# Optimization experiments

Hardware: AMD Instinct MI355X
Metric: run time of the kernel (lower is better)

The kernel has to match this reference:

```python
import jax, jax.numpy as jnp
import numpy as np

NUM_HEADS = 16


def rotate_half(x):
    x1 = x[..., ::2]
    x2 = x[..., 1::2]
    return jnp.concatenate((-x2, x1), axis=-1)


def rope_sin_cos(seq_len, head_dim, dtype):
    inv_freq = 1.0 / (10000.0 ** (jnp.arange(0, head_dim, 2, dtype=jnp.float32) / head_dim))
    t = jnp.arange(seq_len, dtype=jnp.float32)
    freqs = jnp.einsum('i,j->ij', t, inv_freq)          # [S, D/2]
    emb = jnp.concatenate((freqs, freqs), axis=-1)      # [S, D]
    return jnp.sin(emb).astype(dtype), jnp.cos(emb).astype(dtype)


def setup_inputs() -> dict:
    key = jax.random.key(0)
    B, S, E = 2, 2048, 2048
    ks = jax.random.split(key, 5)
    scale = 1.0 / np.sqrt(E)
    return {
        'x': jax.random.normal(ks[0], (B, S, E), dtype=jnp.float32),
        'mask': jnp.ones((B, S), dtype=jnp.int32),
        'Wq': jax.random.normal(ks[1], (E, E), dtype=jnp.float32) * scale,
        'bq': jnp.zeros((E,), dtype=jnp.float32),
        'Wk': jax.random.normal(ks[2], (E, E), dtype=jnp.float32) * scale,
        'bk': jnp.zeros((E,), dtype=jnp.float32),
        'Wv': jax.random.normal(ks[3], (E, E), dtype=jnp.float32) * scale,
        'bv': jnp.zeros((E,), dtype=jnp.float32),
        'Wo': jax.random.normal(ks[4], (E, E), dtype=jnp.float32) * scale,
        'bo': jnp.zeros((E,), dtype=jnp.float32),
    }


def reference(x, mask, Wq, bq, Wk, bk, Wv, bv, Wo, bo):
    B, S, E = x.shape
    H = NUM_HEADS
    D = E // H
    q = (x @ Wq + bq).reshape(B, S, H, D).transpose(0, 2, 1, 3)  # [B,H,S,D]
    k = (x @ Wk + bk).reshape(B, S, H, D).transpose(0, 2, 1, 3)
    v = (x @ Wv + bv).reshape(B, S, H, D).transpose(0, 2, 1, 3)

    sin, cos = rope_sin_cos(S, D, q.dtype)  # [S,D]
    sin = sin[None, None]                    # [1,1,S,D]
    cos = cos[None, None]
    q = q * cos + rotate_half(q) * sin
    k = k * cos + rotate_half(k) * sin

    scores = jnp.einsum('bhqd,bhkd->bhqk', q, k) / jnp.sqrt(jnp.asarray(D, q.dtype))
    scores = jnp.where(mask[:, None, None, :] == 0, -jnp.inf, scores)
    probs = jax.nn.softmax(scores, axis=-1)
    attn = jnp.einsum('bhqk,bhkd->bhqd', probs, v)       # [B,H,S,D]
    attn = attn.transpose(0, 2, 1, 3).reshape(B, S, E)
    return attn @ Wo + bo
```

## Files before the change

### kernel.cpp

```cpp
#include <hip/hip_runtime.h>
#include <hip/hip_bf16.h>
#include <cmath>

typedef unsigned short u16;
typedef unsigned int   u32;

using v4f = __attribute__((ext_vector_type(4))) float;
using s8v = __attribute__((ext_vector_type(8))) short;

union Frag { uint4 u; s8v s; };

__device__ __forceinline__ u16 f2bf(float f){
  u32 u = __float_as_uint(f);
  u32 r = u + 0x7fffu + ((u >> 16) & 1u);
  return (u16)(r >> 16);
}
__device__ __forceinline__ float bf2f(u16 h){ return __uint_as_float(((u32)h) << 16); }

__device__ __forceinline__ void async16(const void* g, void* l){
  __builtin_amdgcn_global_load_lds((__attribute__((address_space(1))) void*)g,
                                   (__attribute__((address_space(3))) void*)l, 16, 0, 0);
}

__global__ __launch_bounds__(256) void cast_x_kernel(const float* __restrict__ x, u16* __restrict__ xb){
  size_t i = ((size_t)blockIdx.x * 256 + threadIdx.x) * 4;
  float4 v = *(const float4*)(x + i);
  uint2 o;
  o.x = (u32)f2bf(v.x) | ((u32)f2bf(v.y) << 16);
  o.y = (u32)f2bf(v.z) | ((u32)f2bf(v.w) << 16);
  *(uint2*)(xb + i) = o;
}

__global__ __launch_bounds__(256) void cast_transpose_kernel(
    const float* __restrict__ W0, const float* __restrict__ W1,
    const float* __restrict__ W2, const float* __restrict__ W3,
    u16* __restrict__ T0, u16* __restrict__ T1, u16* __restrict__ T2, u16* __restrict__ T3){
  __shared__ float tile[64][65];
  const float* W = (blockIdx.z==0)?W0:(blockIdx.z==1)?W1:(blockIdx.z==2)?W2:W3;
  u16*         T = (blockIdx.z==0)?T0:(blockIdx.z==1)?T1:(blockIdx.z==2)?T2:T3;
  const int k0 = blockIdx.y*64, n0 = blockIdx.x*64;
  const int t  = threadIdx.x;
  const int rr = t >> 4, c4 = (t & 15) * 4;
  #pragma unroll
  for (int i=0;i<4;i++){
    int k = rr + i*16;
    float4 v = *(const float4*)(W + (size_t)(k0+k)*2048 + n0 + c4);
    tile[k][c4+0]=v.x; tile[k][c4+1]=v.y; tile[k][c4+2]=v.z; tile[k][c4+3]=v.w;
  }
  __syncthreads();
  #pragma unroll
  for (int i=0;i<4;i++){
    int n = rr + i*16;
    uint2 o;
    o.x = (u32)f2bf(tile[c4+0][n]) | ((u32)f2bf(tile[c4+1][n])<<16);
    o.y = (u32)f2bf(tile[c4+2][n]) | ((u32)f2bf(tile[c4+3][n])<<16);
    *(uint2*)(T + (size_t)(n0+n)*2048 + k0 + c4) = o;
  }
}

template<int MODE>
__global__ __launch_bounds__(256) void gemm_kernel(const u16* __restrict__ A,
                                                   const u16* __restrict__ BT,
                                                   const float* __restrict__ bias,
                                                   void* __restrict__ Cout){
  constexpr int K = 2048;
  __shared__ u16 Asl[128*64];
  __shared__ u16 Bsl[128*64];
  const int tid  = threadIdx.x;
  const int w    = tid >> 6;
  const int lane = tid & 63;
  const int r    = lane & 15, q = lane >> 4;
  const int m0   = blockIdx.y * 128;
  const int n0   = blockIdx.x * 128;
  const int wm   = (w >> 1) * 64, wn = (w & 1) * 64;

  v4f acc[4][4];
  #pragma unroll
  for (int i=0;i<4;i++)
    #pragma unroll
    for (int j=0;j<4;j++) acc[i][j] = (v4f)0.f;

  const int srow = w*32 + (lane>>3);
  const int sblk = (lane&7) ^ ((lane>>3)&7);
  const u16* Ag = A  + (size_t)(m0+srow)*K + sblk*8;
  const u16* Bg = BT + (size_t)(n0+srow)*K + sblk*8;
  u16* Als = Asl + (w*32)*64;
  u16* Bls = Bsl + (w*32)*64;

  for (int kk = 0; kk < K; kk += 64) {
    #pragma unroll
    for (int i=0;i<4;i++){
      async16(Ag + (size_t)i*8*K + kk, Als + i*512);
      async16(Bg + (size_t)i*8*K + kk, Bls + i*512);
    }
    __syncthreads();
    #pragma unroll
    for (int ks=0; ks<2; ++ks) {
      s8v af[4], bfr[4];
      #pragma unroll
      for (int i=0;i<4;i++){
        int rho = wm + i*16 + r;
        int p = (ks*4 + q) ^ (r&7);
        Frag t; t.u = *(const uint4*)(Asl + rho*64 + p*8); af[i] = t.s;
      }
      #pragma unroll
      for (int j=0;j<4;j++){
        int rho = wn + j*16 + r;
        int p = (ks*4 + q) ^ (r&7);
        Frag t; t.u = *(const uint4*)(Bsl + rho*64 + p*8); bfr[j] = t.s;
      }
      #pragma unroll
      for (int i=0;i<4;i++)
        #pragma unroll
        for (int j=0;j<4;j++)
          acc[i][j] = __builtin_amdgcn_mfma_f32_16x16x32_bf16(af[i], bfr[j], acc[i][j], 0, 0, 0);
    }
    __syncthreads();
  }

  float bv[4];
  #pragma unroll
  for (int j=0;j<4;j++) bv[j] = bias[n0 + wn + j*16 + r];

  #pragma unroll
  for (int i=0;i<4;i++){
    #pragma unroll
    for (int j=0;j<4;j++){
      const int gn = n0 + wn + j*16 + r;
      #pragma unroll
      for (int rr2=0; rr2<4; ++rr2){
        const int gm = m0 + wm + i*16 + q*4 + rr2;
        float val = acc[i][j][rr2] + bv[j];
        if (MODE == 0) ((u16*)Cout)[(size_t)gm*2048 + gn] = f2bf(val);
        else           ((float*)Cout)[(size_t)gm*2048 + gn] = val;
      }
    }
  }
}

__global__ __launch_bounds__(256) void rope_kernel(u16* __restrict__ Q, u16* __restrict__ Kb){
  const int wrow = blockIdx.x*4 + (threadIdx.x >> 6);
  const int lane = threadIdx.x & 63;
  u16* P = (blockIdx.y == 0) ? Q : Kb;
  const int s = (wrow >> 4) & 2047;
  const size_t base = (size_t)wrow * 128;
  float invf = exp2f(-(float)lane * 0.20762050593045952f);
  float angle = (float)s * invf;
  float sn, cs;
  sincosf(angle, &sn, &cs);
  float x_j   = bf2f(P[base + lane]);
  float x_j64 = bf2f(P[base + 64 + lane]);
  float x_2j  = bf2f(P[base + 2*lane]);
  float x_2j1 = bf2f(P[base + 2*lane + 1]);
  float o0 = x_j  * cs - x_2j1 * sn;
  float o1 = x_j64 * cs + x_2j  * sn;
  P[base + lane]      = f2bf(o0);
  P[base + 64 + lane] = f2bf(o1);
}

__global__ __launch_bounds__(256) void transpose_v_kernel(const u16* __restrict__ V, u16* __restrict__ VT){
  __shared__ u16 t[64*72];
  const int s0 = blockIdx.x*64;
  const int d0 = blockIdx.y*64;
  const int bh = blockIdx.z;
  const int b = bh >> 4, h = bh & 15;
  const size_t obase = ((size_t)bh*128 + d0)*2048 + s0;
  const int tid = threadIdx.x;
  #pragma unroll
  for (int i=0;i<2;i++){
    int c = tid + i*256;
    int sl = c >> 3, dc = (c & 7) * 8;
    *(uint4*)(t + sl*72 + dc) =
      *(const uint4*)(V + ((size_t)(b*2048 + s0 + sl))*2048 + h*128 + d0 + dc);
  }
  __syncthreads();
  #pragma unroll
  for (int i=0;i<2;i++){
    int c = tid + i*256;
    int dl = c >> 3, sc4 = (c & 7) * 8;
    u16 tmp[8];
    #pragma unroll
    for (int j=0;j<8;j++) tmp[j] = t[(sc4+j)*72 + dl];
    *(uint4*)(VT + obase + (size_t)dl*2048 + sc4) = *(const uint4*)tmp;
  }
}

__global__ __launch_bounds__(256,4) void attn_kernel(const u16* __restrict__ Q,
                                                     const u16* __restrict__ K,
                                                     const u16* __restrict__ VT,
                                                     const int* __restrict__ mask,
                                                     u16* __restrict__ Out){
  constexpr int S = 2048;
  constexpr float SL2 = 0.08838834764831845f * 1.4426950408889634f;
  __shared__ u16 smem[20480];
  u16* KQlds = smem;
  u16* Vlds  = smem + 8192;
  u16* Plds  = smem + 16384;

  const int tid = threadIdx.x, w = tid >> 6, lane = tid & 63;
  const int r = lane & 15, q = lane >> 4;
  const int h = blockIdx.y, b = blockIdx.z;
  const int q0 = blockIdx.x * 64;
  const size_t rowb = (size_t)b * 2048;
  const size_t bhD  = ((size_t)(b*16 + h)) * 128;

  const int sr4 = lane >> 4;
  const int sp16 = lane & 15;
  #pragma unroll
  for (int i=0;i<4;i++){
    int R = w*16 + i*4;
    int blk = sp16 ^ ((R&7) + sr4);
    async16(Q + (rowb + q0 + R + sr4)*2048 + h*128 + blk*8, KQlds + R*128);
  }
  __syncthreads();
  s8v qf[4];
  #pragma unroll
  for (int kc=0;kc<4;kc++){
    int rho = w*16 + r;
    int p = (kc*4 + q) ^ (r&7);
    Frag t; t.u = *(const uint4*)(KQlds + rho*128 + p*8);
    qf[kc] = t.s;
  }
  __syncthreads();

  v4f accO[8];
  #pragma unroll
  for (int n=0;n<8;n++) accO[n] = (v4f)0.f;
  float lsum[4] = {0.f, 0.f, 0.f, 0.f};

  u16* Pw = Plds + w*1024;

  const int vr8 = lane >> 3;
  const int vblk = (lane&7) ^ ((lane>>3)&7);

  for (int it=0; it<32; ++it){
    const int key0 = it*64;
    #pragma unroll
    for (int i=0;i<4;i++){
      int R = w*16 + i*4;
      int blk = sp16 ^ ((R&7) + sr4);
      async16(K + (rowb + key0 + R + sr4)*2048 + h*128 + blk*8, KQlds + R*128);
    }
    #pragma unroll
    for (int i=0;i<4;i++){
      int R = w*32 + i*8;
      async16(VT + (bhD + R + vr8)*2048 + key0 + vblk*8, Vlds + R*64);
    }
    __syncthreads();

    v4f sc[4];
    #pragma unroll
    for (int n=0;n<4;n++){
      v4f a = (v4f)0.f;
      #pragma unroll
      for (int kc=0;kc<4;kc++){
        int rho = n*16 + r;
        int p = (kc*4 + q) ^ (r&7);
        Frag t; t.u = *(const uint4*)(KQlds + rho*128 + p*8);
        a = __builtin_amdgcn_mfma_f32_16x16x32_bf16(qf[kc], t.s, a, 0, 0, 0);
      }
      sc[n] = a;
    }

    int mv[4];
    #pragma unroll
    for (int n=0;n<4;n++) mv[n] = mask[b*S + key0 + n*16 + r];

    #pragma unroll
    for (int g=0;g<4;g++){
      const int row = q*4 + g;
      const int rb = row*64 + (r&7);
      #pragma unroll
      for (int n=0;n<4;n++){
        float p = exp2f(sc[n][g] * SL2);
        if (mv[n] == 0) p = 0.f;
        lsum[g] += p;
        int pp = (n*2 + (r>>3)) ^ (row&7);
        Pw[rb + pp*8] = f2bf(p);
      }
    }

    #pragma unroll
    for (int kc=0;kc<2;kc++){
      int p = (kc*4 + q) ^ (r&7);
      Frag tp; tp.u = *(const uint4*)(Pw + r*64 + p*8);
      #pragma unroll
      for (int n=0;n<8;n++){
        int d = n*16 + r;
        Frag tv; tv.u = *(const uint4*)(Vlds + d*64 + p*8);
        accO[n] = __builtin_amdgcn_mfma_f32_16x16x32_bf16(tp.s, tv.s, accO[n], 0, 0, 0);
      }
    }
    __syncthreads();
  }

  float inv[4];
  #pragma unroll
  for (int g=0;g<4;g++){
    float s = lsum[g];
    #pragma unroll
    for (int off=1; off<16; off<<=1) s += __shfl_xor(s, off, 64);
    inv[g] = (s > 0.f) ? 1.f/s : 0.f;
  }

  #pragma unroll
  for (int n=0;n<8;n++){
    #pragma unroll
    for (int g=0;g<4;g++){
      int s = q0 + w*16 + q*4 + g;
      int col = h*128 + n*16 + r;
      Out[(rowb + s)*2048 + col] = f2bf(accO[n][g] * inv[g]);
    }
  }
}

extern "C" void kernel_launch(void* const* d_in, const int* in_sizes, int n_in,
                              void* d_out, int out_size, void* d_ws, size_t ws_size,
                              hipStream_t stream) {
  (void)in_sizes; (void)n_in; (void)out_size; (void)ws_size;
  const float* x    = (const float*)d_in[0];
  const int*   mask = (const int*)d_in[1];
  const float* Wq   = (const float*)d_in[2];
  const float* bq   = (const float*)d_in[3];
  const float* Wk   = (const float*)d_in[4];
  const float* bk   = (const float*)d_in[5];
  const float* Wv   = (const float*)d_in[6];
  const float* bv   = (const float*)d_in[7];
  const float* Wo   = (const float*)d_in[8];
  const float* bo   = (const float*)d_in[9];

  u16* xbf = (u16*)d_ws;
  u16* WqT = xbf + 8388608;
  u16* WkT = WqT + 4194304;
  u16* WvT = WkT + 4194304;
  u16* WoT = WvT + 4194304;
  u16* Qb  = WoT + 4194304;
  u16* Kb  = Qb + 8388608;
  u16* Vb  = Kb + 8388608;
  u16* Ab  = Vb + 8388608;
  u16* VTb = Ab + 8388608;

  cast_x_kernel<<<8192, 256, 0, stream>>>(x, xbf);
  cast_transpose_kernel<<<dim3(32,32,4), 256, 0, stream>>>(Wq, Wk, Wv, Wo, WqT, WkT, WvT, WoT);
  gemm_kernel<0><<<dim3(16,32), 256, 0, stream>>>(xbf, WqT, bq, Qb);
  gemm_kernel<0><<<dim3(16,32), 256, 0, stream>>>(xbf, WkT, bk, Kb);
  gemm_kernel<0><<<dim3(16,32), 256, 0, stream>>>(xbf, WvT, bv, Vb);
  rope_kernel<<<dim3(16384,2), 256, 0, stream>>>(Qb, Kb);
  transpose_v_kernel<<<dim3(32,2,32), 256, 0, stream>>>(Vb, VTb);
  attn_kernel<<<dim3(32,16,2), 256, 0, stream>>>(Qb, Kb, VTb, mask, Ab);
  gemm_kernel<1><<<dim3(16,32), 256, 0, stream>>>(Ab, WoT, bo, (float*)d_out);
}
```

Baseline: 446.5 us.

## Rewrite attention with 32x32 MFMA, register-resident P via permlane swaps

The attention kernel moves from 16x16x32 to 32x32x16 MFMA tiles and computes S^T = K·Q^T, so each wave owns 32 query rows and a block covers 128 queries. Probabilities are packed to bf16 and rearranged with permlane32_swap to feed the PV MFMA directly, which removes the P round-trip through LDS. The mask becomes a per-tile ballot that skips per-element masking when every key is valid. Q fragments now load straight from global memory, and occupancy drops to 2 blocks per SIMD with half as many blocks, which may reduce latency hiding.

Result: faster. 428.9 us (-4.0%).

```diff
diff --git a/kernel.cpp b/kernel.cpp
--- a/kernel.cpp
+++ b/kernel.cpp
@@ -5,8 +5,10 @@
 typedef unsigned short u16;
 typedef unsigned int   u32;
 
-using v4f = __attribute__((ext_vector_type(4))) float;
-using s8v = __attribute__((ext_vector_type(8))) short;
+using v4f    = __attribute__((ext_vector_type(4)))  float;
+using f32x16 = __attribute__((ext_vector_type(16))) float;
+using s8v    = __attribute__((ext_vector_type(8)))  short;
+using u32x2  = __attribute__((ext_vector_type(2)))  unsigned int;
 
 union Frag { uint4 u; s8v s; };
 
@@ -16,6 +18,9 @@
   return (u16)(r >> 16);
 }
 __device__ __forceinline__ float bf2f(u16 h){ return __uint_as_float(((u32)h) << 16); }
+__device__ __forceinline__ u32 pkbf(float a, float b){
+  return (u32)f2bf(a) | ((u32)f2bf(b) << 16);
+}
 
 __device__ __forceinline__ void async16(const void* g, void* l){
   __builtin_amdgcn_global_load_lds((__attribute__((address_space(1))) void*)g,
@@ -185,131 +190,110 @@
   }
 }
 
-__global__ __launch_bounds__(256,4) void attn_kernel(const u16* __restrict__ Q,
+__global__ __launch_bounds__(256,2) void attn_kernel(const u16* __restrict__ Q,
                                                      const u16* __restrict__ K,
                                                      const u16* __restrict__ VT,
                                                      const int* __restrict__ mask,
                                                      u16* __restrict__ Out){
   constexpr int S = 2048;
   constexpr float SL2 = 0.08838834764831845f * 1.4426950408889634f;
-  __shared__ u16 smem[20480];
-  u16* KQlds = smem;
-  u16* Vlds  = smem + 8192;
-  u16* Plds  = smem + 16384;
+  __shared__ u16 smem[16384];
+  u16* Ks = smem;
+  u16* Vs = smem + 8192;
 
   const int tid = threadIdx.x, w = tid >> 6, lane = tid & 63;
-  const int r = lane & 15, q = lane >> 4;
-  const int h = blockIdx.y, b = blockIdx.z;
-  const int q0 = blockIdx.x * 64;
+  const int qc = lane & 31;
+  const int h  = lane >> 5;
+  const int l7 = lane & 7;
+  const int hh = blockIdx.y, b = blockIdx.z;
+  const int q0 = blockIdx.x * 128;
   const size_t rowb = (size_t)b * 2048;
-  const size_t bhD  = ((size_t)(b*16 + h)) * 128;
-
-  const int sr4 = lane >> 4;
-  const int sp16 = lane & 15;
-  #pragma unroll
-  for (int i=0;i<4;i++){
-    int R = w*16 + i*4;
-    int blk = sp16 ^ ((R&7) + sr4);
-    async16(Q + (rowb + q0 + R + sr4)*2048 + h*128 + blk*8, KQlds + R*128);
-  }
-  __syncthreads();
-  s8v qf[4];
-  #pragma unroll
-  for (int kc=0;kc<4;kc++){
-    int rho = w*16 + r;
-    int p = (kc*4 + q) ^ (r&7);
-    Frag t; t.u = *(const uint4*)(KQlds + rho*128 + p*8);
-    qf[kc] = t.s;
-  }
-  __syncthreads();
-
-  v4f accO[8];
-  #pragma unroll
-  for (int n=0;n<8;n++) accO[n] = (v4f)0.f;
-  float lsum[4] = {0.f, 0.f, 0.f, 0.f};
-
-  u16* Pw = Plds + w*1024;
-
-  const int vr8 = lane >> 3;
-  const int vblk = (lane&7) ^ ((lane>>3)&7);
+  const size_t bhD  = ((size_t)(b*16 + hh)) * 128;
+
+  s8v qf[8];
+  {
+    const u16* qp = Q + (rowb + q0 + w*32 + qc)*2048 + hh*128 + h*8;
+    #pragma unroll
+    for (int t=0;t<8;t++){ Frag f; f.u = *(const uint4*)(qp + t*16); qf[t] = f.s; }
+  }
+
+  f32x16 accO[4];
+  #pragma unroll
+  for (int d=0; d<4; d++) accO[d] = (f32x16)0.f;
+  float lsum = 0.f;
+
+  const int sr4 = lane >> 4, sp16 = lane & 15;
+  const int vr8 = lane >> 3, vp8 = lane & 7;
 
   for (int it=0; it<32; ++it){
     const int key0 = it*64;
     #pragma unroll
     for (int i=0;i<4;i++){
       int R = w*16 + i*4;
-      int blk = sp16 ^ ((R&7) + sr4);
-      async16(K + (rowb + key0 + R + sr4)*2048 + h*128 + blk*8, KQlds + R*128);
+      int ob = sp16 ^ ((R&7) + sr4);
+      async16(K + (rowb + key0 + R + sr4)*2048 + hh*128 + ob*8, Ks + R*128);
     }
     #pragma unroll
     for (int i=0;i<4;i++){
       int R = w*32 + i*8;
-      async16(VT + (bhD + R + vr8)*2048 + key0 + vblk*8, Vlds + R*64);
-    }
+      int ob = vp8 ^ vr8;
+      async16(VT + (bhD + R + vr8)*2048 + key0 + ob*8, Vs + R*64);
+    }
+    unsigned long long bm = __ballot(mask[b*S + key0 + lane] != 0);
     __syncthreads();
 
-    v4f sc[4];
-    #pragma unroll
-    for (int n=0;n<4;n++){
-      v4f a = (v4f)0.f;
-      #pragma unroll
-      for (int kc=0;kc<4;kc++){
-        int rho = n*16 + r;
-        int p = (kc*4 + q) ^ (r&7);
-        Frag t; t.u = *(const uint4*)(KQlds + rho*128 + p*8);
-        a = __builtin_amdgcn_mfma_f32_16x16x32_bf16(qf[kc], t.s, a, 0, 0, 0);
-      }
-      sc[n] = a;
-    }
-
-    int mv[4];
-    #pragma unroll
-    for (int n=0;n<4;n++) mv[n] = mask[b*S + key0 + n*16 + r];
-
-    #pragma unroll
-    for (int g=0;g<4;g++){
-      const int row = q*4 + g;
-      const int rb = row*64 + (r&7);
-      #pragma unroll
-      for (int n=0;n<4;n++){
-        float p = exp2f(sc[n][g] * SL2);
-        if (mv[n] == 0) p = 0.f;
-        lsum[g] += p;
-        int pp = (n*2 + (r>>3)) ^ (row&7);
-        Pw[rb + pp*8] = f2bf(p);
-      }
-    }
-
-    #pragma unroll
-    for (int kc=0;kc<2;kc++){
-      int p = (kc*4 + q) ^ (r&7);
-      Frag tp; tp.u = *(const uint4*)(Pw + r*64 + p*8);
-      #pragma unroll
-      for (int n=0;n<8;n++){
-        int d = n*16 + r;
-        Frag tv; tv.u = *(const uint4*)(Vlds + d*64 + p*8);
-        accO[n] = __builtin_amdgcn_mfma_f32_16x16x32_bf16(tp.s, tv.s, accO[n], 0, 0, 0);
+    #pragma unroll
+    for (int nb=0; nb<2; ++nb){
+      f32x16 sc = (f32x16)0.f;
+      #pragma unroll
+      for (int t=0;t<8;t++){
+        Frag kf; kf.u = *(const uint4*)(Ks + (nb*32 + qc)*128 + (((2*t + h) ^ l7)*8));
+        sc = __builtin_amdgcn_mfma_f32_32x32x16_bf16(kf.s, qf[t], sc, 0, 0, 0);
+      }
+      float p[16];
+      #pragma unroll
+      for (int m=0; m<16; ++m) p[m] = exp2f(sc[m] * SL2);
+      if (bm != ~0ull){
+        #pragma unroll
+        for (int m=0; m<16; ++m){
+          int bit = nb*32 + (m&3) + 8*(m>>2) + 4*h;
+          if (!((bm >> bit) & 1ull)) p[m] = 0.f;
+        }
+      }
+      #pragma unroll
+      for (int m=0; m<16; ++m) lsum += p[m];
+
+      #pragma unroll
+      for (int g=0; g<2; ++g){
+        u32 a0 = pkbf(p[8*g+0], p[8*g+1]);
+        u32 a1 = pkbf(p[8*g+2], p[8*g+3]);
+        u32 a2 = pkbf(p[8*g+4], p[8*g+5]);
+        u32 a3 = pkbf(p[8*g+6], p[8*g+7]);
+        u32x2 r0 = __builtin_amdgcn_permlane32_swap(a0, a2, false, false);
+        u32x2 r1 = __builtin_amdgcn_permlane32_swap(a1, a3, false, false);
+        Frag pf; pf.u = make_uint4(r0[0], r1[0], r0[1], r1[1]);
+        const int T = nb*2 + g;
+        #pragma unroll
+        for (int d=0; d<4; ++d){
+          Frag vf; vf.u = *(const uint4*)(Vs + (d*32 + qc)*64 + (((2*T + h) ^ l7)*8));
+          accO[d] = __builtin_amdgcn_mfma_f32_32x32x16_bf16(vf.s, pf.s, accO[d], 0, 0, 0);
+        }
       }
     }
     __syncthreads();
   }
 
-  float inv[4];
-  #pragma unroll
-  for (int g=0;g<4;g++){
-    float s = lsum[g];
-    #pragma unroll
-    for (int off=1; off<16; off<<=1) s += __shfl_xor(s, off, 64);
-    inv[g] = (s > 0.f) ? 1.f/s : 0.f;
-  }
-
-  #pragma unroll
-  for (int n=0;n<8;n++){
-    #pragma unroll
-    for (int g=0;g<4;g++){
-      int s = q0 + w*16 + q*4 + g;
-      int col = h*128 + n*16 + r;
-      Out[(rowb + s)*2048 + col] = f2bf(accO[n][g] * inv[g]);
+  float sall = lsum + __shfl_xor(lsum, 32, 64);
+  float invv = (sall > 0.f) ? 1.f/sall : 0.f;
+  u16* orow = Out + (rowb + q0 + w*32 + qc)*2048 + hh*128;
+  #pragma unroll
+  for (int d=0; d<4; ++d){
+    #pragma unroll
+    for (int g2=0; g2<4; ++g2){
+      union { u16 q4[4]; uint2 u; } o;
+      #pragma unroll
+      for (int j=0;j<4;j++) o.q4[j] = f2bf(accO[d][g2*4+j] * invv);
+      *(uint2*)(orow + d*32 + g2*8 + 4*h) = o.u;
     }
   }
 }
@@ -347,6 +331,6 @@
   gemm_kernel<0><<<dim3(16,32), 256, 0, stream>>>(xbf, WvT, bv, Vb);
   rope_kernel<<<dim3(16384,2), 256, 0, stream>>>(Qb, Kb);
   transpose_v_kernel<<<dim3(32,2,32), 256, 0, stream>>>(Vb, VTb);
-  attn_kernel<<<dim3(32,16,2), 256, 0, stream>>>(Qb, Kb, VTb, mask, Ab);
+  attn_kernel<<<dim3(16,16,2), 256, 0, stream>>>(Qb, Kb, VTb, mask, Ab);
   gemm_kernel<1><<<dim3(16,32), 256, 0, stream>>>(Ab, WoT, bo, (float*)d_out);
 }
```
